# Optimization experiments

Measured on AMD Instinct MI355X. Metric: run time of the kernel, lower is better.

Reference implementation:

```python
import jax, jax.numpy as jnp
import numpy as np

D, H, Wd, V, OUTF = 256, 512, 512, 32, 256


def setup_inputs() -> dict:
    key = jax.random.key(0)
    k1, k2, k3, k4 = jax.random.split(key, 4)
    X = jax.random.normal(k1, (1, D, H, Wd), dtype=jnp.float32)
    W = jax.random.normal(k2, (D, V), dtype=jnp.float32)
    # variance is divided by; keep it bounded away from zero
    variance = jax.random.uniform(k3, (D, V), dtype=jnp.float32, minval=0.5, maxval=1.5)
    weight = jax.random.normal(k4, (D, OUTF), dtype=jnp.float32) * 0.05
    return {"X": X, "W": W, "variance": variance, "weight": weight}


def reference(X, W, variance, weight):
    _, d, h, w = X.shape
    outf = weight.shape[1]
    # torch does reshape(X, (h, w, d)) -> flatten to (h*w, d); plain reshape, faithful
    Xf = jnp.reshape(X, (h * w, d))
    iv = 1.0 / variance          # (d, V)
    iv2 = iv * iv
    # Q[p,i] = sum_d ((x_pd - W_di) / var_di)^2, expanded into 2 GEMMs + bias
    Q = (Xf * Xf) @ iv2 - 2.0 * (Xf @ (W * iv2)) + jnp.sum(W * W * iv2, axis=0)[None, :]
    Q = Q - jnp.min(Q, axis=1, keepdims=True)
    Q = jnp.exp(-0.5 * Q)
    Q = Q / jnp.sum(Q, axis=1, keepdims=True)      # (hw, V) row-stochastic
    s = jnp.sum(Q, axis=0)                          # (V,)
    # Z[:,i] = sum_p Q_pi * (x_p - W[:,i]) / var[:,i] / s_i
    Z = ((Xf.T @ Q) - W * s[None, :]) * iv / s[None, :]   # (d, V)
    # original divides by sum of squares (not its sqrt) -- keep faithful
    Z = Z / jnp.sum(Z * Z, axis=0, keepdims=True)
    Adj = Z.T @ Z                                   # (V, V)
    Zo = jax.nn.relu(Adj @ (Z.T @ weight))          # (V, outf)
    Xn = Q @ Zo                                     # (hw, outf)
    # torch: reshape (h, w, outf) then .view(1, outf, h, w) == plain reshape
    return jnp.reshape(Xn, (1, outf, h, w))
```

## Files before the change

### kernel.cpp

```cpp
#include <hip/hip_runtime.h>

#define D_    256
#define V_    32
#define HW_   (512*512)
#define OUTF_ 256

__global__ __launch_bounds__(256) void k1_q(const float* __restrict__ X,
                                            const float* __restrict__ W,
                                            const float* __restrict__ var,
                                            float* __restrict__ Q,
                                            float* __restrict__ s_out)
{
    __shared__ float As[D_][V_];
    __shared__ float Bs[D_][V_];
    const int tid = threadIdx.x;

    {
        const float* wr = W   + tid * V_;
        const float* vr = var + tid * V_;
        #pragma unroll
        for (int i = 0; i < V_; ++i) {
            float iv = 1.0f / vr[i];
            As[tid][i] = wr[i] * iv;
            Bs[tid][i] = iv;
        }
    }
    __syncthreads();

    const size_t pA = (size_t)blockIdx.x * 512 + tid;
    const size_t pB = pA + 256;
    const float4* xrowA = (const float4*)(X + pA * D_);
    const float4* xrowB = (const float4*)(X + pB * D_);

    float tA[V_], tB[V_];
    #pragma unroll
    for (int i = 0; i < V_; ++i) { tA[i] = 0.f; tB[i] = 0.f; }

    for (int d4 = 0; d4 < D_/4; ++d4) {
        float4 xa = xrowA[d4];
        float4 xb = xrowB[d4];
        float xsa[4] = {xa.x, xa.y, xa.z, xa.w};
        float xsb[4] = {xb.x, xb.y, xb.z, xb.w};
        #pragma unroll
        for (int k = 0; k < 4; ++k) {
            const int d = d4*4 + k;
            const float xA = xsa[k];
            const float xB = xsb[k];
            #pragma unroll
            for (int i = 0; i < V_; ++i) {
                const float bi = Bs[d][i];
                const float ai = As[d][i];
                float eA = fmaf(xA, bi, -ai);
                float eB = fmaf(xB, bi, -ai);
                tA[i] = fmaf(eA, eA, tA[i]);
                tB[i] = fmaf(eB, eB, tB[i]);
            }
        }
    }

    float qA[V_], qB[V_];
    float mnA = 3.4e38f, mnB = 3.4e38f;
    #pragma unroll
    for (int i = 0; i < V_; ++i) { mnA = fminf(mnA, tA[i]); mnB = fminf(mnB, tB[i]); }
    float sumA = 0.f, sumB = 0.f;
    #pragma unroll
    for (int i = 0; i < V_; ++i) {
        qA[i] = __expf(-0.5f * (tA[i] - mnA));  sumA += qA[i];
        qB[i] = __expf(-0.5f * (tB[i] - mnB));  sumB += qB[i];
    }
    const float invA = 1.0f / sumA;
    const float invB = 1.0f / sumB;

    float4* qoutA = (float4*)(Q + pA * V_);
    float4* qoutB = (float4*)(Q + pB * V_);
    #pragma unroll
    for (int j = 0; j < V_/4; ++j) {
        float4 oa, ob;
        oa.x = qA[4*j+0]*invA; oa.y = qA[4*j+1]*invA; oa.z = qA[4*j+2]*invA; oa.w = qA[4*j+3]*invA;
        ob.x = qB[4*j+0]*invB; ob.y = qB[4*j+1]*invB; ob.z = qB[4*j+2]*invB; ob.w = qB[4*j+3]*invB;
        qoutA[j] = oa;
        qoutB[j] = ob;
    }

    __syncthreads();
    float* s_blk = &As[0][0];
    if (tid < V_) s_blk[tid] = 0.f;
    __syncthreads();
    #pragma unroll
    for (int i = 0; i < V_; ++i) {
        atomicAdd(&s_blk[i], qA[i]*invA + qB[i]*invB);
    }
    __syncthreads();
    if (tid < V_) atomicAdd(&s_out[tid], s_blk[tid]);
}

__global__ __launch_bounds__(256) void k2_m(const float* __restrict__ X,
                                            const float* __restrict__ Q,
                                            float* __restrict__ M)
{
    const int d = threadIdx.x;
    const size_t p0 = (size_t)blockIdx.x * 512;
    float acc[V_];
    #pragma unroll
    for (int i = 0; i < V_; ++i) acc[i] = 0.f;

    for (int pp = 0; pp < 512; ++pp) {
        const size_t p = p0 + pp;
        const float x = X[p * D_ + d];
        const float* qr = Q + p * V_;
        #pragma unroll
        for (int i = 0; i < V_; ++i) acc[i] = fmaf(x, qr[i], acc[i]);
    }
    #pragma unroll
    for (int i = 0; i < V_; ++i) atomicAdd(&M[d*V_ + i], acc[i]);
}

__global__ __launch_bounds__(256) void k3a(const float* __restrict__ M,
                                           const float* __restrict__ s_in,
                                           const float* __restrict__ W,
                                           const float* __restrict__ var,
                                           float* __restrict__ Z,
                                           float* __restrict__ Adj)
{
    __shared__ float Zl[D_][V_];
    __shared__ float ss[V_];
    __shared__ float nrm[V_];
    const int t = threadIdx.x;
    if (t < V_) ss[t] = s_in[t];
    __syncthreads();

    #pragma unroll
    for (int i = 0; i < V_; ++i) {
        float iv = 1.0f / var[t*V_ + i];
        float z = (M[t*V_ + i] - W[t*V_ + i] * ss[i]) * iv / ss[i];
        Zl[t][i] = z;
    }
    __syncthreads();
    if (t < V_) {
        float n = 0.f;
        for (int d = 0; d < D_; ++d) { float z = Zl[d][t]; n = fmaf(z, z, n); }
        nrm[t] = n;
    }
    __syncthreads();
    #pragma unroll
    for (int i = 0; i < V_; ++i) {
        float z = Zl[t][i] / nrm[i];
        Zl[t][i] = z;
        Z[t*V_ + i] = z;
    }
    __syncthreads();
    #pragma unroll
    for (int e = 0; e < 4; ++e) {
        int idx = t*4 + e;
        int i = idx >> 5, j = idx & 31;
        float a = 0.f;
        for (int d = 0; d < D_; ++d) a = fmaf(Zl[d][i], Zl[d][j], a);
        Adj[idx] = a;
    }
}

__global__ __launch_bounds__(256) void k3b(const float* __restrict__ Z,
                                           const float* __restrict__ weight,
                                           const float* __restrict__ Adj,
                                           float* __restrict__ Zo)
{
    __shared__ float T[V_];
    const int t = threadIdx.x;
    const int f = blockIdx.x;
    if (t < V_) T[t] = 0.f;
    __syncthreads();
    const float wt = weight[t*OUTF_ + f];
    const float* zr = Z + t*V_;
    #pragma unroll
    for (int j = 0; j < V_; ++j) atomicAdd(&T[j], zr[j] * wt);
    __syncthreads();
    if (t < V_) {
        float o = 0.f;
        #pragma unroll
        for (int j = 0; j < V_; ++j) o = fmaf(Adj[t*V_ + j], T[j], o);
        Zo[t*OUTF_ + f] = fmaxf(o, 0.f);
    }
}

__global__ __launch_bounds__(256) void k4_out(const float* __restrict__ Q,
                                              const float* __restrict__ Zo,
                                              float* __restrict__ out)
{
    __shared__ float Qt[256][V_];
    const int t = threadIdx.x;
    const size_t p0 = (size_t)blockIdx.x * 256;

    float zc[V_];
    #pragma unroll
    for (int i = 0; i < V_; ++i) zc[i] = Zo[i*OUTF_ + t];

    {
        float4* dst = (float4*)(&Qt[t][0]);
        const float4* src = (const float4*)(Q + (p0 + t) * V_);
        #pragma unroll
        for (int j = 0; j < V_/4; ++j) dst[j] = src[j];
    }
    __syncthreads();

    #pragma unroll 2
    for (int p = 0; p < 256; ++p) {
        float a0 = 0.f, a1 = 0.f, a2 = 0.f, a3 = 0.f;
        #pragma unroll
        for (int i = 0; i < V_; i += 4) {
            a0 = fmaf(Qt[p][i+0], zc[i+0], a0);
            a1 = fmaf(Qt[p][i+1], zc[i+1], a1);
            a2 = fmaf(Qt[p][i+2], zc[i+2], a2);
            a3 = fmaf(Qt[p][i+3], zc[i+3], a3);
        }
        out[(p0 + p) * OUTF_ + t] = (a0 + a1) + (a2 + a3);
    }
}

extern "C" void kernel_launch(void* const* d_in, const int* in_sizes, int n_in,
                              void* d_out, int out_size, void* d_ws, size_t ws_size,
                              hipStream_t stream)
{
    const float* X      = (const float*)d_in[0];
    const float* W      = (const float*)d_in[1];
    const float* var    = (const float*)d_in[2];
    const float* weight = (const float*)d_in[3];
    float* out = (float*)d_out;
    float* ws  = (float*)d_ws;

    float* Q   = ws;
    float* s   = Q   + (size_t)HW_ * V_;
    float* M   = s   + V_;
    float* Z   = M   + D_ * V_;
    float* Adj = Z   + D_ * V_;
    float* Zo  = Adj + V_ * V_;

    hipMemsetAsync(s, 0, (V_ + D_*V_) * sizeof(float), stream);

    k1_q <<<HW_/512, 256, 0, stream>>>(X, W, var, Q, s);
    k2_m <<<HW_/512, 256, 0, stream>>>(X, Q, M);
    k3a  <<<1,       256, 0, stream>>>(M, s, W, var, Z, Adj);
    k3b  <<<OUTF_,   256, 0, stream>>>(Z, weight, Adj, Zo);
    k4_out<<<HW_/256, 256, 0, stream>>>(Q, Zo, out);
}
```

Measured before the change: 1.155 ms.

## Stage Q tiles in LDS for k2 and register-block 4 features in k4

k2 now copies each block's Q rows into a double-buffered LDS tile with coalesced float4 loads and reads them as LDS broadcasts, replacing the per-thread scalar global reads of Q. k4 splits the block into four wavefront groups of 64 pixels each, and each thread computes four adjacent output features with float4 stores. The whole Q tile is loaded coalesced into LDS. This is meant to raise arithmetic reuse and memory coalescing in the two bandwidth-heavy kernels, at the cost of more registers per thread (128 zc values in k4).

Measured after the change: 1.190 ms. +3.0%, slower.

```diff
diff --git a/kernel.cpp b/kernel.cpp
--- a/kernel.cpp
+++ b/kernel.cpp
@@ -94,25 +94,57 @@
     if (tid < V_) atomicAdd(&s_out[tid], s_blk[tid]);
 }
 
+#define K2_PXB   512
+#define K2_CHUNK 128
+
 __global__ __launch_bounds__(256) void k2_m(const float* __restrict__ X,
                                             const float* __restrict__ Q,
                                             float* __restrict__ M)
 {
-    const int d = threadIdx.x;
-    const size_t p0 = (size_t)blockIdx.x * 512;
+    __shared__ __align__(16) float Qs[2][K2_CHUNK][V_];
+    const int t = threadIdx.x;
+    const size_t p0 = (size_t)blockIdx.x * K2_PXB;
+
     float acc[V_];
     #pragma unroll
     for (int i = 0; i < V_; ++i) acc[i] = 0.f;
 
-    for (int pp = 0; pp < 512; ++pp) {
-        const size_t p = p0 + pp;
-        const float x = X[p * D_ + d];
-        const float* qr = Q + p * V_;
-        #pragma unroll
-        for (int i = 0; i < V_; ++i) acc[i] = fmaf(x, qr[i], acc[i]);
-    }
-    #pragma unroll
-    for (int i = 0; i < V_; ++i) atomicAdd(&M[d*V_ + i], acc[i]);
+    {
+        const float4* src = (const float4*)(Q + p0 * V_);
+        float4* dst = (float4*)(&Qs[0][0][0]);
+        #pragma unroll
+        for (int k = 0; k < 4; ++k) dst[t + 256*k] = src[t + 256*k];
+    }
+
+    for (int c = 0; c < K2_PXB/K2_CHUNK; ++c) {
+        __syncthreads();
+        if (c + 1 < K2_PXB/K2_CHUNK) {
+            const float4* src = (const float4*)(Q + (p0 + (size_t)(c+1)*K2_CHUNK) * V_);
+            float4* dst = (float4*)(&Qs[(c+1)&1][0][0]);
+            #pragma unroll
+            for (int k = 0; k < 4; ++k) dst[t + 256*k] = src[t + 256*k];
+        }
+
+        const float* xb = X + (p0 + (size_t)c*K2_CHUNK) * D_ + t;
+        const float (*qb)[V_] = Qs[c&1];
+
+        #pragma unroll 16
+        for (int pp = 0; pp < K2_CHUNK; ++pp) {
+            const float x = xb[(size_t)pp * D_];
+            const float4* q4 = (const float4*)(&qb[pp][0]);
+            #pragma unroll
+            for (int j = 0; j < 8; ++j) {
+                float4 q = q4[j];
+                acc[4*j+0] = fmaf(x, q.x, acc[4*j+0]);
+                acc[4*j+1] = fmaf(x, q.y, acc[4*j+1]);
+                acc[4*j+2] = fmaf(x, q.z, acc[4*j+2]);
+                acc[4*j+3] = fmaf(x, q.w, acc[4*j+3]);
+            }
+        }
+    }
+
+    #pragma unroll
+    for (int i = 0; i < V_; ++i) atomicAdd(&M[t*V_ + i], acc[i]);
 }
 
 __global__ __launch_bounds__(256) void k3a(const float* __restrict__ M,
@@ -186,33 +218,55 @@
                                               const float* __restrict__ Zo,
                                               float* __restrict__ out)
 {
-    __shared__ float Qt[256][V_];
-    const int t = threadIdx.x;
+    __shared__ __align__(16) float Qt[256][V_];
+    const int t  = threadIdx.x;
+    const int fq = t & 63;
+    const int w  = t >> 6;
     const size_t p0 = (size_t)blockIdx.x * 256;
 
-    float zc[V_];
-    #pragma unroll
-    for (int i = 0; i < V_; ++i) zc[i] = Zo[i*OUTF_ + t];
+    float zc[4][V_];
+    #pragma unroll
+    for (int i = 0; i < V_; ++i) {
+        float4 z = ((const float4*)(Zo + i*OUTF_))[fq];
+        zc[0][i] = z.x; zc[1][i] = z.y; zc[2][i] = z.z; zc[3][i] = z.w;
+    }
 
     {
-        float4* dst = (float4*)(&Qt[t][0]);
-        const float4* src = (const float4*)(Q + (p0 + t) * V_);
-        #pragma unroll
-        for (int j = 0; j < V_/4; ++j) dst[j] = src[j];
-    }
-    __syncthreads();
-
+        float4* dst = (float4*)(&Qt[0][0]);
+        const float4* src = (const float4*)(Q + p0 * V_);
+        #pragma unroll
+        for (int k = 0; k < 8; ++k) dst[t + 256*k] = src[t + 256*k];
+    }
+    __syncthreads();
+
+    float4* out4 = (float4*)(out + (p0 + (size_t)w*64) * OUTF_);
     #pragma unroll 2
-    for (int p = 0; p < 256; ++p) {
+    for (int pp = 0; pp < 64; ++pp) {
+        const int p = w*64 + pp;
+        const float4* q4 = (const float4*)(&Qt[p][0]);
         float a0 = 0.f, a1 = 0.f, a2 = 0.f, a3 = 0.f;
         #pragma unroll
-        for (int i = 0; i < V_; i += 4) {
-            a0 = fmaf(Qt[p][i+0], zc[i+0], a0);
-            a1 = fmaf(Qt[p][i+1], zc[i+1], a1);
-            a2 = fmaf(Qt[p][i+2], zc[i+2], a2);
-            a3 = fmaf(Qt[p][i+3], zc[i+3], a3);
-        }
-        out[(p0 + p) * OUTF_ + t] = (a0 + a1) + (a2 + a3);
+        for (int j = 0; j < 8; ++j) {
+            float4 q = q4[j];
+            a0 = fmaf(q.x, zc[0][4*j+0], a0);
+            a1 = fmaf(q.x, zc[1][4*j+0], a1);
+            a2 = fmaf(q.x, zc[2][4*j+0], a2);
+            a3 = fmaf(q.x, zc[3][4*j+0], a3);
+            a0 = fmaf(q.y, zc[0][4*j+1], a0);
+            a1 = fmaf(q.y, zc[1][4*j+1], a1);
+            a2 = fmaf(q.y, zc[2][4*j+1], a2);
+            a3 = fmaf(q.y, zc[3][4*j+1], a3);
+            a0 = fmaf(q.z, zc[0][4*j+2], a0);
+            a1 = fmaf(q.z, zc[1][4*j+2], a1);
+            a2 = fmaf(q.z, zc[2][4*j+2], a2);
+            a3 = fmaf(q.z, zc[3][4*j+2], a3);
+            a0 = fmaf(q.w, zc[0][4*j+3], a0);
+            a1 = fmaf(q.w, zc[1][4*j+3], a1);
+            a2 = fmaf(q.w, zc[2][4*j+3], a2);
+            a3 = fmaf(q.w, zc[3][4*j+3], a3);
+        }
+        float4 o; o.x = a0; o.y = a1; o.z = a2; o.w = a3;
+        out4[pp*64 + fq] = o;
     }
 }
 
```
